# Kernel tuning notes

Hardware: AMD Instinct MI355X
Metric: run time of the kernel (lower is better)

The kernel has to match this reference:

```python
import jax, jax.numpy as jnp
import numpy as np
import math

D = 768
SCALE = math.sqrt(D)


def setup_inputs() -> dict:
    key = jax.random.key(0)
    k1, k2, k3, k4 = jax.random.split(key, 4)
    lhs = jax.random.normal(k1, (8, 1024, D), dtype=jnp.float32)
    rhs = jax.random.normal(k2, (8, 1024, D), dtype=jnp.float32)
    # xavier_normal_ std = sqrt(2/(fan_in+fan_out))
    std = math.sqrt(2.0 / (D + D))
    W_lhs = jax.random.normal(k3, (D, D), dtype=jnp.float32) * std
    W_rhs = jax.random.normal(k4, (D, D), dtype=jnp.float32) * std
    return {"lhs": lhs, "rhs": rhs, "W_lhs": W_lhs, "W_rhs": W_rhs}


def reference(lhs, rhs, W_lhs, W_rhs):
    # Linear (no bias): x @ W.T, then tanh
    l = jnp.tanh(jnp.einsum('nld,ed->nle', lhs, W_lhs))  # (N, L, D)
    r = jnp.tanh(jnp.einsum('nrd,ed->nre', rhs, W_rhs))  # (N, R, D)
    scores = jnp.einsum('nld,nrd->nlr', l, r)            # (N, L, R)
    attn_lhs = jax.nn.softmax(scores, axis=2)            # unscaled, row softmax
    attn_rhs = jax.nn.softmax(scores / SCALE, axis=1)    # scaled, column softmax
    out_lhs = jnp.einsum('nlr,nrd->nld', attn_lhs, rhs)
    out_rhs = jnp.einsum('nlr,nld->nrd', attn_rhs, lhs)
    return (jnp.concatenate([lhs, out_lhs], axis=2),
            jnp.concatenate([rhs, out_rhs], axis=2))
```

## Files before the change

kernel.cpp:

```cpp
#include <hip/hip_runtime.h>

typedef _Float16 f16_t;
typedef _Float16 f16x4 __attribute__((ext_vector_type(4)));
typedef _Float16 f16x8 __attribute__((ext_vector_type(8)));
typedef short s16x8 __attribute__((ext_vector_type(8)));
typedef float floatx4 __attribute__((ext_vector_type(4)));

#define NB 8
#define SEQ 1024
#define DIM 768
#define INV_SCALE 0.03608439182435161f
#define ROW_SHIFT 40.0f

__device__ inline unsigned short f2bf(float f) {
  unsigned u = __builtin_bit_cast(unsigned, f);
  u += 0x7fffu + ((u >> 16) & 1u);
  return (unsigned short)(u >> 16);
}

__device__ inline void async_load16(const void* g, void* l) {
  __builtin_amdgcn_global_load_lds((__attribute__((address_space(1))) void*)g,
                                   (__attribute__((address_space(3))) void*)l,
                                   16, 0, 0);
}


__global__ __launch_bounds__(256, 3) void gemm_proj(
    const f16_t* __restrict__ A0, const f16_t* __restrict__ W0,
    const f16_t* __restrict__ A1, const f16_t* __restrict__ W1,
    f16_t* __restrict__ C0, f16_t* __restrict__ C1) {
  __shared__ __align__(16) f16_t sA[128 * 64];
  __shared__ __align__(16) f16_t sB[128 * 64];
  const int b = blockIdx.x;
  const int n = b & 7;
  const int s = b >> 3;
  const int side = s / 48;
  const int t = s - side * 48;
  const int myb = t / 6, j = t - myb * 6;
  const int my = n * 8 + myb;
  const f16_t* Ab = (side ? A1 : A0) + (size_t)my * 128 * DIM;
  const f16_t* Bb = (side ? W1 : W0) + (size_t)j * 128 * DIM;
  f16_t* C = side ? C1 : C0;
  const int tid = threadIdx.x;
  const int lane = tid & 63;
  const int wave = tid >> 6;
  const int wr = wave >> 1, wc = wave & 1;
  const int fr = lane & 15;
  const int fq = lane >> 4;
  const int swz = ((lane & 7) ^ (lane >> 3)) << 3;
  const int x7 = (fr & 7) << 3;

  floatx4 acc[4][4] = {};

  for (int kt = 0; kt < DIM; kt += 64) {
    #pragma unroll
    for (int i = 0; i < 4; ++i) {
      const int ch = i * 4 + wave;
      const int row = ch * 8 + (lane >> 3);
      const size_t g = (size_t)row * DIM + kt + swz;
      async_load16(Ab + g, (char*)sA + ch * 1024);
      async_load16(Bb + g, (char*)sB + ch * 1024);
    }
    __syncthreads();
    #pragma unroll
    for (int ks = 0; ks < 64; ks += 32) {
      f16x8 af[4], bf[4];
      #pragma unroll
      for (int t2 = 0; t2 < 4; ++t2) {
        const int cs = (ks + fq * 8) ^ x7;
        af[t2] = *(const f16x8*)&sA[(wr * 64 + t2 * 16 + fr) * 64 + cs];
        bf[t2] = *(const f16x8*)&sB[(wc * 64 + t2 * 16 + fr) * 64 + cs];
      }
      #pragma unroll
      for (int ti = 0; ti < 4; ++ti)
        #pragma unroll
        for (int tj = 0; tj < 4; ++tj)
          acc[ti][tj] = __builtin_amdgcn_mfma_f32_16x16x32_f16(
              af[ti], bf[tj], acc[ti][tj], 0, 0, 0);
    }
    __syncthreads();
  }

  const size_t m0 = (size_t)my * 128, n0 = (size_t)j * 128;
  #pragma unroll
  for (int ti = 0; ti < 4; ++ti)
    #pragma unroll
    for (int tj = 0; tj < 4; ++tj) {
      const size_t gm = m0 + wr * 64 + ti * 16 + fq * 4;
      const size_t gn = n0 + wc * 64 + tj * 16 + fr;
      #pragma unroll
      for (int i = 0; i < 4; ++i) {
        const float e = __expf(2.f * acc[ti][tj][i]);
        C[(gm + i) * DIM + gn] =
            (f16_t)(1.f - 2.f * __builtin_amdgcn_rcpf(e + 1.f));
      }
    }
}

__global__ __launch_bounds__(256, 3) void scores_mix(
    const f16_t* __restrict__ A, const f16_t* __restrict__ B,
    const float* __restrict__ lhs32, const float* __restrict__ rhs32,
    unsigned short* __restrict__ e_l, f16_t* __restrict__ e_rT,
    f16_t* __restrict__ lhsT, unsigned short* __restrict__ rhsT,
    float* __restrict__ rowpart, float* __restrict__ colpart) {
  __shared__ __align__(16) char smem[32768];
  const int b = blockIdx.x;
  const int tid = threadIdx.x;

  if (b >= 512) {
    float(*tile)[65] = (float(*)[65])smem;
    const int t = b - 512;
    const int side = t >> 7;
    const int n = (t >> 4) & 7, r0 = (t & 15) * 64;
    const float* in = (side ? rhs32 : lhs32) + (size_t)n * SEQ * DIM;
    const int x = tid & 63, y = tid >> 6;
    for (int d0 = 0; d0 < DIM; d0 += 64) {
      #pragma unroll
      for (int yy = y; yy < 64; yy += 4)
        tile[yy][x] = in[(size_t)(r0 + yy) * DIM + d0 + x];
      __syncthreads();
      if (side == 0) {
        f16_t* out = lhsT + (size_t)n * SEQ * DIM;
        #pragma unroll
        for (int yy = y; yy < 64; yy += 4)
          out[(size_t)(d0 + yy) * SEQ + r0 + x] = (f16_t)tile[x][yy];
      } else {
        unsigned short* out = rhsT + (size_t)n * SEQ * DIM;
        #pragma unroll
        for (int yy = y; yy < 64; yy += 4)
          out[(size_t)(d0 + yy) * SEQ + r0 + x] = f2bf(tile[x][yy]);
      }
      __syncthreads();
    }
    return;
  }

  f16_t* sA = (f16_t*)smem;
  f16_t* sB = sA + 8192;
  const int z = b & 7;
  const int s = b >> 3;
  const int my = s >> 3, j = s & 7;
  const f16_t* Ab = A + (size_t)z * SEQ * DIM + (size_t)my * 128 * DIM;
  const f16_t* Bb = B + (size_t)z * SEQ * DIM + (size_t)j * 128 * DIM;
  const int lane = tid & 63;
  const int wave = tid >> 6;
  const int wr = wave >> 1, wc = wave & 1;
  const int fr = lane & 15;
  const int fq = lane >> 4;
  const int swz = ((lane & 7) ^ (lane >> 3)) << 3;
  const int x7 = (fr & 7) << 3;

  floatx4 acc[4][4] = {};

  for (int kt = 0; kt < DIM; kt += 64) {
    #pragma unroll
    for (int i = 0; i < 4; ++i) {
      const int ch = i * 4 + wave;
      const int row = ch * 8 + (lane >> 3);
      const size_t g = (size_t)row * DIM + kt + swz;
      async_load16(Ab + g, (char*)sA + ch * 1024);
      async_load16(Bb + g, (char*)sB + ch * 1024);
    }
    __syncthreads();
    #pragma unroll
    for (int ks = 0; ks < 64; ks += 32) {
      f16x8 af[4], bf[4];
      #pragma unroll
      for (int t2 = 0; t2 < 4; ++t2) {
        const int cs = (ks + fq * 8) ^ x7;
        af[t2] = *(const f16x8*)&sA[(wr * 64 + t2 * 16 + fr) * 64 + cs];
        bf[t2] = *(const f16x8*)&sB[(wc * 64 + t2 * 16 + fr) * 64 + cs];
      }
      #pragma unroll
      for (int ti = 0; ti < 4; ++ti)
        #pragma unroll
        for (int tj = 0; tj < 4; ++tj)
          acc[ti][tj] = __builtin_amdgcn_mfma_f32_16x16x32_f16(
              af[ti], bf[tj], acc[ti][tj], 0, 0, 0);
    }
    __syncthreads();
  }

  const size_t m0 = (size_t)my * 128, n0 = (size_t)j * 128;
  unsigned short* eL = e_l + (size_t)z * SEQ * SEQ;
  f16_t* eT = e_rT + (size_t)z * SEQ * SEQ;

  #pragma unroll
  for (int ti = 0; ti < 4; ++ti) {
    #pragma unroll
    for (int i = 0; i < 4; ++i) {
      const int rloc = wr * 64 + ti * 16 + fq * 4 + i;
      float sum = 0.f;
      #pragma unroll
      for (int tj = 0; tj < 4; ++tj) {
        const float e = __expf(acc[ti][tj][i] - ROW_SHIFT);
        sum += e;
        eL[(m0 + rloc) * SEQ + n0 + wc * 64 + tj * 16 + fr] = f2bf(e);
      }
      sum += __shfl_xor(sum, 1, 64);
      sum += __shfl_xor(sum, 2, 64);
      sum += __shfl_xor(sum, 4, 64);
      sum += __shfl_xor(sum, 8, 64);
      if (fr == 0)
        rowpart[((size_t)(z * 16 + j * 2 + wc)) * SEQ + m0 + rloc] = sum;
    }
  }
  #pragma unroll
  for (int tj = 0; tj < 4; ++tj) {
    const int rp = wc * 64 + tj * 16 + fr;
    float sum = 0.f;
    #pragma unroll
    for (int ti = 0; ti < 4; ++ti) {
      #pragma unroll
      for (int i = 0; i < 4; ++i) {
        const float e = __expf(acc[ti][tj][i] * INV_SCALE);
        sum += e;
        const int cp = wr * 64 + ti * 16 + fq * 4 + i;
        *(f16_t*)(smem + rp * 256 + ((cp * 2) ^ ((rp & 7) << 4))) = (f16_t)e;
      }
    }
    sum += __shfl_xor(sum, 16, 64);
    sum += __shfl_xor(sum, 32, 64);
    if (fq == 0)
      colpart[((size_t)(z * 16 + my * 2 + wr)) * SEQ + n0 + rp] = sum;
  }
  __syncthreads();
  #pragma unroll
  for (int it = 0; it < 8; ++it) {
    const int r = it * 16 + (tid >> 4), chunk = tid & 15;
    const f16x8 v =
        *(const f16x8*)(smem + r * 256 + ((chunk * 16) ^ ((r & 7) << 4)));
    *(f16x8*)&eT[(n0 + r) * SEQ + m0 + chunk * 8] = v;
  }
}

template <bool BF>
__device__ __forceinline__ void apply_body(
    const f16_t* __restrict__ Ab, const f16_t* __restrict__ Bb,
    float* __restrict__ C, const float* __restrict__ pp, f16_t* sA, f16_t* sB,
    float* sinv) {
  const int tid = threadIdx.x;
  const int lane = tid & 63;
  const int wave = tid >> 6;
  const int wr = wave >> 1, wc = wave & 1;
  const int fr = lane & 15;
  const int fq = lane >> 4;
  const int swz = ((lane & 7) ^ (lane >> 3)) << 3;
  const int x7 = (fr & 7) << 3;

  if (tid < 128) {
    float s = 0.f;
    #pragma unroll
    for (int k = 0; k < 16; ++k) s += pp[k * SEQ + tid];
    sinv[tid] = 1.f / s;
  }

  floatx4 acc[4][4] = {};

  for (int kt = 0; kt < SEQ; kt += 64) {
    #pragma unroll
    for (int i = 0; i < 4; ++i) {
      const int ch = i * 4 + wave;
      const int row = ch * 8 + (lane >> 3);
      const size_t g = (size_t)row * SEQ + kt + swz;
      async_load16(Ab + g, (char*)sA + ch * 1024);
      async_load16(Bb + g, (char*)sB + ch * 1024);
    }
    __syncthreads();
    #pragma unroll
    for (int ks = 0; ks < 64; ks += 32) {
      const int cs = (ks + fq * 8) ^ x7;
      #pragma unroll
      for (int ti = 0; ti < 4; ++ti) {
        const f16_t* pa = &sA[(wr * 64 + ti * 16 + fr) * 64 + cs];
        #pragma unroll
        for (int tj = 0; tj < 4; ++tj) {
          const f16_t* pb = &sB[(wc * 64 + tj * 16 + fr) * 64 + cs];
          if constexpr (BF)
            acc[ti][tj] = __builtin_amdgcn_mfma_f32_16x16x32_bf16(
                *(const s16x8*)pa, *(const s16x8*)pb, acc[ti][tj], 0, 0, 0);
          else
            acc[ti][tj] = __builtin_amdgcn_mfma_f32_16x16x32_f16(
                *(const f16x8*)pa, *(const f16x8*)pb, acc[ti][tj], 0, 0, 0);
        }
      }
    }
    __syncthreads();
  }

  #pragma unroll
  for (int ti = 0; ti < 4; ++ti) {
    const int gm = wr * 64 + ti * 16 + fq * 4;
    const floatx4 iv = *(const floatx4*)&sinv[gm];
    #pragma unroll
    for (int tj = 0; tj < 4; ++tj) {
      const int gn = wc * 64 + tj * 16 + fr;
      #pragma unroll
      for (int i = 0; i < 4; ++i)
        C[(size_t)(gm + i) * (2 * DIM) + gn] = acc[ti][tj][i] * iv[i];
    }
  }
}

__global__ __launch_bounds__(256, 3) void gemm_apply(
    const f16_t* __restrict__ e_l, const f16_t* __restrict__ e_rT,
    const f16_t* __restrict__ rhsT, const f16_t* __restrict__ lhsT,
    const float* __restrict__ rowpart, const float* __restrict__ colpart,
    float* __restrict__ out0, float* __restrict__ out1) {
  __shared__ __align__(16) f16_t sA[128 * 64];
  __shared__ __align__(16) f16_t sB[128 * 64];
  __shared__ __align__(16) float sinv[128];
  const int b = blockIdx.x;
  const int n = b & 7;
  const int s = b >> 3;
  const int side = s / 48;
  const int t = s - side * 48;
  const int my = t / 6, j = t - my * 6;
  const size_t m0 = (size_t)my * 128, n0 = (size_t)j * 128;
  if (side == 0) {
    apply_body<true>(e_l + (size_t)n * SEQ * SEQ + m0 * SEQ,
                     rhsT + (size_t)n * SEQ * DIM + n0 * SEQ,
                     out0 + (size_t)n * SEQ * 2 * DIM + DIM + m0 * 2 * DIM + n0,
                     rowpart + (size_t)n * 16 * SEQ + m0, sA, sB, sinv);
  } else {
    apply_body<false>(
        e_rT + (size_t)n * SEQ * SEQ + m0 * SEQ,
        lhsT + (size_t)n * SEQ * DIM + n0 * SEQ,
        out1 + (size_t)n * SEQ * 2 * DIM + DIM + m0 * 2 * DIM + n0,
        colpart + (size_t)n * 16 * SEQ + m0, sA, sB, sinv);
  }
}

__global__ __launch_bounds__(256) void prep(
    const float* __restrict__ lhs, const float* __restrict__ rhs,
    const float* __restrict__ Wl, const float* __restrict__ Wr,
    f16_t* __restrict__ lf, f16_t* __restrict__ rf, f16_t* __restrict__ Wlh,
    f16_t* __restrict__ Wrh, float* __restrict__ o0, float* __restrict__ o1) {
  const int which = blockIdx.y;
  const int bx = blockIdx.x;
  if (bx >= 6144) {
    const float4* in = (const float4*)(which ? Wr : Wl);
    f16_t* out = which ? Wrh : Wlh;
    const int idx = (bx - 6144) * 256 + threadIdx.x;
    const float4 v = in[idx];
    f16x4 h = {(f16_t)v.x, (f16_t)v.y, (f16_t)v.z, (f16_t)v.w};
    *(f16x4*)(out + idx * 4) = h;
    return;
  }
  const float4* in = (const float4*)(which ? rhs : lhs);
  f16_t* out = which ? rf : lf;
  float* outh = which ? o1 : o0;
  const int idx = bx * 256 + threadIdx.x;
  const float4 v = in[idx];
  const int i4 = idx * 4;
  f16x4 h = {(f16_t)v.x, (f16_t)v.y, (f16_t)v.z, (f16_t)v.w};
  *(f16x4*)(out + i4) = h;
  const int row = i4 / DIM, col = i4 % DIM;
  *(float4*)&outh[(size_t)row * (2 * DIM) + col] = v;
}

extern "C" void kernel_launch(void* const* d_in, const int* in_sizes, int n_in,
                              void* d_out, int out_size, void* d_ws,
                              size_t ws_size, hipStream_t stream) {
  const float* lhs = (const float*)d_in[0];
  const float* rhs = (const float*)d_in[1];
  const float* Wl = (const float*)d_in[2];
  const float* Wr = (const float*)d_in[3];
  float* out0 = (float*)d_out;
  float* out1 = out0 + (size_t)NB * SEQ * (2 * DIM);

  char* ws = (char*)d_ws;
  f16_t* lhsT = (f16_t*)(ws + 0);
  unsigned short* rhsT = (unsigned short*)(ws + 12582912);
  f16_t* l_f = (f16_t*)(ws + 25165824);
  f16_t* r_f = (f16_t*)(ws + 37748736);
  f16_t* lhs_f = (f16_t*)(ws + 50331648);
  f16_t* rhs_f = (f16_t*)(ws + 62914560);
  f16_t* Wl_h = (f16_t*)(ws + 75497472);
  f16_t* Wr_h = (f16_t*)(ws + 76677120);
  unsigned short* e_l = (unsigned short*)(ws + 50331648);
  f16_t* e_rT = (f16_t*)(ws + 67108864);
  float* rowpart = (float*)(ws + 83886080);
  float* colpart = (float*)(ws + 84410368);

  prep<<<dim3(6720, 2), 256, 0, stream>>>(lhs, rhs, Wl, Wr, lhs_f, rhs_f,
                                          Wl_h, Wr_h, out0, out1);
  gemm_proj<<<768, 256, 0, stream>>>(lhs_f, Wl_h, rhs_f, Wr_h, l_f, r_f);
  scores_mix<<<768, 256, 0, stream>>>(l_f, r_f, lhs, rhs, e_l, e_rT, lhsT,
                                      rhsT, rowpart, colpart);
  gemm_apply<<<768, 256, 0, stream>>>((const f16_t*)e_l, e_rT,
                                      (const f16_t*)rhsT, lhsT, rowpart,
                                      colpart, out0, out1);
}
```

Before: 242.8 us.

## Fuse fp32-to-fp16 conversion into projection GEMM and drop prep kernel

The separate prep kernel, which converted inputs and weights to fp16 and copied the passthrough halves of the outputs, is removed. The projection GEMM now loads fp32 tiles directly with vector loads, converts them in registers and writes swizzled fp16 into LDS. The passthrough copy moves into the transpose blocks of scores_mix. This removes one launch and a full fp16 round trip through memory. In exchange the GEMM loses its async global-to-LDS loads, reads twice as many bytes per tile, and spends extra VALU work on conversion.

```diff
diff --git a/kernel.cpp b/kernel.cpp
--- a/kernel.cpp
+++ b/kernel.cpp
@@ -26,8 +26,8 @@
 
 
 __global__ __launch_bounds__(256, 3) void gemm_proj(
-    const f16_t* __restrict__ A0, const f16_t* __restrict__ W0,
-    const f16_t* __restrict__ A1, const f16_t* __restrict__ W1,
+    const float* __restrict__ A0, const float* __restrict__ W0,
+    const float* __restrict__ A1, const float* __restrict__ W1,
     f16_t* __restrict__ C0, f16_t* __restrict__ C1) {
   __shared__ __align__(16) f16_t sA[128 * 64];
   __shared__ __align__(16) f16_t sB[128 * 64];
@@ -38,8 +38,8 @@
   const int t = s - side * 48;
   const int myb = t / 6, j = t - myb * 6;
   const int my = n * 8 + myb;
-  const f16_t* Ab = (side ? A1 : A0) + (size_t)my * 128 * DIM;
-  const f16_t* Bb = (side ? W1 : W0) + (size_t)j * 128 * DIM;
+  const float* Ab = (side ? A1 : A0) + (size_t)my * 128 * DIM;
+  const float* Bb = (side ? W1 : W0) + (size_t)j * 128 * DIM;
   f16_t* C = side ? C1 : C0;
   const int tid = threadIdx.x;
   const int lane = tid & 63;
@@ -47,19 +47,24 @@
   const int wr = wave >> 1, wc = wave & 1;
   const int fr = lane & 15;
   const int fq = lane >> 4;
-  const int swz = ((lane & 7) ^ (lane >> 3)) << 3;
   const int x7 = (fr & 7) << 3;
+  const int c4 = tid & 15;
+  const int rq = tid >> 4;
 
   floatx4 acc[4][4] = {};
 
   for (int kt = 0; kt < DIM; kt += 64) {
     #pragma unroll
-    for (int i = 0; i < 4; ++i) {
-      const int ch = i * 4 + wave;
-      const int row = ch * 8 + (lane >> 3);
-      const size_t g = (size_t)row * DIM + kt + swz;
-      async_load16(Ab + g, (char*)sA + ch * 1024);
-      async_load16(Bb + g, (char*)sB + ch * 1024);
+    for (int p = 0; p < 8; ++p) {
+      const int row = p * 16 + rq;
+      const int dst =
+          row * 64 + (((c4 >> 1) ^ (row & 7)) << 3) + ((c4 & 1) << 2);
+      const float4 va = *(const float4*)&Ab[(size_t)row * DIM + kt + c4 * 4];
+      const float4 vb = *(const float4*)&Bb[(size_t)row * DIM + kt + c4 * 4];
+      *(f16x4*)&sA[dst] =
+          f16x4{(f16_t)va.x, (f16_t)va.y, (f16_t)va.z, (f16_t)va.w};
+      *(f16x4*)&sB[dst] =
+          f16x4{(f16_t)vb.x, (f16_t)vb.y, (f16_t)vb.z, (f16_t)vb.w};
     }
     __syncthreads();
     #pragma unroll
@@ -102,7 +107,8 @@
     const float* __restrict__ lhs32, const float* __restrict__ rhs32,
     unsigned short* __restrict__ e_l, f16_t* __restrict__ e_rT,
     f16_t* __restrict__ lhsT, unsigned short* __restrict__ rhsT,
-    float* __restrict__ rowpart, float* __restrict__ colpart) {
+    float* __restrict__ rowpart, float* __restrict__ colpart,
+    float* __restrict__ out0, float* __restrict__ out1) {
   __shared__ __align__(16) char smem[32768];
   const int b = blockIdx.x;
   const int tid = threadIdx.x;
@@ -113,11 +119,15 @@
     const int side = t >> 7;
     const int n = (t >> 4) & 7, r0 = (t & 15) * 64;
     const float* in = (side ? rhs32 : lhs32) + (size_t)n * SEQ * DIM;
+    float* oh = (side ? out1 : out0) + (size_t)n * SEQ * 2 * DIM;
     const int x = tid & 63, y = tid >> 6;
     for (int d0 = 0; d0 < DIM; d0 += 64) {
       #pragma unroll
-      for (int yy = y; yy < 64; yy += 4)
-        tile[yy][x] = in[(size_t)(r0 + yy) * DIM + d0 + x];
+      for (int yy = y; yy < 64; yy += 4) {
+        const float v = in[(size_t)(r0 + yy) * DIM + d0 + x];
+        tile[yy][x] = v;
+        oh[(size_t)(r0 + yy) * (2 * DIM) + d0 + x] = v;
+      }
       __syncthreads();
       if (side == 0) {
         f16_t* out = lhsT + (size_t)n * SEQ * DIM;
@@ -331,34 +341,6 @@
   }
 }
 
-__global__ __launch_bounds__(256) void prep(
-    const float* __restrict__ lhs, const float* __restrict__ rhs,
-    const float* __restrict__ Wl, const float* __restrict__ Wr,
-    f16_t* __restrict__ lf, f16_t* __restrict__ rf, f16_t* __restrict__ Wlh,
-    f16_t* __restrict__ Wrh, float* __restrict__ o0, float* __restrict__ o1) {
-  const int which = blockIdx.y;
-  const int bx = blockIdx.x;
-  if (bx >= 6144) {
-    const float4* in = (const float4*)(which ? Wr : Wl);
-    f16_t* out = which ? Wrh : Wlh;
-    const int idx = (bx - 6144) * 256 + threadIdx.x;
-    const float4 v = in[idx];
-    f16x4 h = {(f16_t)v.x, (f16_t)v.y, (f16_t)v.z, (f16_t)v.w};
-    *(f16x4*)(out + idx * 4) = h;
-    return;
-  }
-  const float4* in = (const float4*)(which ? rhs : lhs);
-  f16_t* out = which ? rf : lf;
-  float* outh = which ? o1 : o0;
-  const int idx = bx * 256 + threadIdx.x;
-  const float4 v = in[idx];
-  const int i4 = idx * 4;
-  f16x4 h = {(f16_t)v.x, (f16_t)v.y, (f16_t)v.z, (f16_t)v.w};
-  *(f16x4*)(out + i4) = h;
-  const int row = i4 / DIM, col = i4 % DIM;
-  *(float4*)&outh[(size_t)row * (2 * DIM) + col] = v;
-}
-
 extern "C" void kernel_launch(void* const* d_in, const int* in_sizes, int n_in,
                               void* d_out, int out_size, void* d_ws,
                               size_t ws_size, hipStream_t stream) {
@@ -374,20 +356,14 @@
   unsigned short* rhsT = (unsigned short*)(ws + 12582912);
   f16_t* l_f = (f16_t*)(ws + 25165824);
   f16_t* r_f = (f16_t*)(ws + 37748736);
-  f16_t* lhs_f = (f16_t*)(ws + 50331648);
-  f16_t* rhs_f = (f16_t*)(ws + 62914560);
-  f16_t* Wl_h = (f16_t*)(ws + 75497472);
-  f16_t* Wr_h = (f16_t*)(ws + 76677120);
   unsigned short* e_l = (unsigned short*)(ws + 50331648);
   f16_t* e_rT = (f16_t*)(ws + 67108864);
   float* rowpart = (float*)(ws + 83886080);
   float* colpart = (float*)(ws + 84410368);
 
-  prep<<<dim3(6720, 2), 256, 0, stream>>>(lhs, rhs, Wl, Wr, lhs_f, rhs_f,
-                                          Wl_h, Wr_h, out0, out1);
-  gemm_proj<<<768, 256, 0, stream>>>(lhs_f, Wl_h, rhs_f, Wr_h, l_f, r_f);
+  gemm_proj<<<768, 256, 0, stream>>>(lhs, Wl, rhs, Wr, l_f, r_f);
   scores_mix<<<768, 256, 0, stream>>>(l_f, r_f, lhs, rhs, e_l, e_rT, lhsT,
-                                      rhsT, rowpart, colpart);
+                                      rhsT, rowpart, colpart, out0, out1);
   gemm_apply<<<768, 256, 0, stream>>>((const f16_t*)e_l, e_rT,
                                       (const f16_t*)rhsT, lhsT, rowpart,
                                       colpart, out0, out1);
```

Measured after the change: 267.1 us. 1.1x slower.

## Fuse input transposes into prep kernel and reorder GEMM tile mapping

Applied to the files above, without the earlier changes.

Folds the lhs/rhs transpose (to fp16 and bf16 transposed copies) into the prep kernel, so each fp32 input is read once instead of twice. Prep now works on 64x64 tiles with a padded shared-memory tile. The scores kernel becomes a pure GEMM launched with fewer blocks. Block indexing in the projection and apply kernels now makes consecutive blocks share the same column tile, which should improve cache reuse of the weight and B operands. The cost is a heavier prep kernel with shared-memory transposes and the loss of the overlap the transpose previously had with the scores GEMM.

```diff
diff --git a/kernel.cpp b/kernel.cpp
--- a/kernel.cpp
+++ b/kernel.cpp
@@ -4,6 +4,7 @@
 typedef _Float16 f16x4 __attribute__((ext_vector_type(4)));
 typedef _Float16 f16x8 __attribute__((ext_vector_type(8)));
 typedef short s16x8 __attribute__((ext_vector_type(8)));
+typedef unsigned short u16x4 __attribute__((ext_vector_type(4)));
 typedef float floatx4 __attribute__((ext_vector_type(4)));
 
 #define NB 8
@@ -24,6 +25,68 @@
                                    16, 0, 0);
 }
 
+
+__global__ __launch_bounds__(256) void prep(
+    const float* __restrict__ lhs, const float* __restrict__ rhs,
+    const float* __restrict__ Wl, const float* __restrict__ Wr,
+    f16_t* __restrict__ lf, f16_t* __restrict__ rf, f16_t* __restrict__ lhsT,
+    unsigned short* __restrict__ rhsT, f16_t* __restrict__ Wlh,
+    f16_t* __restrict__ Wrh, float* __restrict__ o0, float* __restrict__ o1) {
+  const int z = blockIdx.z;
+  const int tid = threadIdx.x;
+  const int x4 = (tid & 15) * 4, ty = tid >> 4;
+  const int c0 = blockIdx.x * 64, r0 = blockIdx.y * 64;
+  if (z >= 16) {
+    if (blockIdx.y >= 12) return;
+    const float* in = (z == 17 ? Wr : Wl);
+    f16_t* out = (z == 17 ? Wrh : Wlh);
+    #pragma unroll
+    for (int it = 0; it < 4; ++it) {
+      const int row = r0 + ty + it * 16;
+      const float4 v = *(const float4*)&in[(size_t)row * DIM + c0 + x4];
+      f16x4 h = {(f16_t)v.x, (f16_t)v.y, (f16_t)v.z, (f16_t)v.w};
+      *(f16x4*)&out[(size_t)row * DIM + c0 + x4] = h;
+    }
+    return;
+  }
+  __shared__ float tile[64][65];
+  const int n = z & 7;
+  const float* in = (z < 8 ? lhs : rhs) + (size_t)n * SEQ * DIM;
+  f16_t* fout = (z < 8 ? lf : rf) + (size_t)n * SEQ * DIM;
+  float* oh = (z < 8 ? o0 : o1) + (size_t)n * SEQ * 2 * DIM;
+  #pragma unroll
+  for (int it = 0; it < 4; ++it) {
+    const int row = ty + it * 16;
+    const float4 v = *(const float4*)&in[(size_t)(r0 + row) * DIM + c0 + x4];
+    f16x4 h = {(f16_t)v.x, (f16_t)v.y, (f16_t)v.z, (f16_t)v.w};
+    *(f16x4*)&fout[(size_t)(r0 + row) * DIM + c0 + x4] = h;
+    *(float4*)&oh[(size_t)(r0 + row) * 2 * DIM + c0 + x4] = v;
+    tile[row][x4 + 0] = v.x;
+    tile[row][x4 + 1] = v.y;
+    tile[row][x4 + 2] = v.z;
+    tile[row][x4 + 3] = v.w;
+  }
+  __syncthreads();
+  if (z < 8) {
+    f16_t* T = lhsT + (size_t)n * SEQ * DIM;
+    #pragma unroll
+    for (int it = 0; it < 4; ++it) {
+      const int cr = ty + it * 16;
+      f16x4 o = {(f16_t)tile[x4 + 0][cr], (f16_t)tile[x4 + 1][cr],
+                 (f16_t)tile[x4 + 2][cr], (f16_t)tile[x4 + 3][cr]};
+      *(f16x4*)&T[(size_t)(c0 + cr) * SEQ + r0 + x4] = o;
+    }
+  } else {
+    unsigned short* T = rhsT + (size_t)n * SEQ * DIM;
+    #pragma unroll
+    for (int it = 0; it < 4; ++it) {
+      const int cr = ty + it * 16;
+      u16x4 o = {f2bf(tile[x4 + 0][cr]), f2bf(tile[x4 + 1][cr]),
+                 f2bf(tile[x4 + 2][cr]), f2bf(tile[x4 + 3][cr])};
+      *(u16x4*)&T[(size_t)(c0 + cr) * SEQ + r0 + x4] = o;
+    }
+  }
+}
 
 __global__ __launch_bounds__(256, 3) void gemm_proj(
     const f16_t* __restrict__ A0, const f16_t* __restrict__ W0,
@@ -36,7 +99,7 @@
   const int s = b >> 3;
   const int side = s / 48;
   const int t = s - side * 48;
-  const int myb = t / 6, j = t - myb * 6;
+  const int j = t >> 3, myb = t & 7;
   const int my = n * 8 + myb;
   const f16_t* Ab = (side ? A1 : A0) + (size_t)my * 128 * DIM;
   const f16_t* Bb = (side ? W1 : W0) + (size_t)j * 128 * DIM;
@@ -97,44 +160,13 @@
     }
 }
 
-__global__ __launch_bounds__(256, 3) void scores_mix(
+__global__ __launch_bounds__(256, 3) void gemm_scores(
     const f16_t* __restrict__ A, const f16_t* __restrict__ B,
-    const float* __restrict__ lhs32, const float* __restrict__ rhs32,
     unsigned short* __restrict__ e_l, f16_t* __restrict__ e_rT,
-    f16_t* __restrict__ lhsT, unsigned short* __restrict__ rhsT,
     float* __restrict__ rowpart, float* __restrict__ colpart) {
   __shared__ __align__(16) char smem[32768];
   const int b = blockIdx.x;
   const int tid = threadIdx.x;
-
-  if (b >= 512) {
-    float(*tile)[65] = (float(*)[65])smem;
-    const int t = b - 512;
-    const int side = t >> 7;
-    const int n = (t >> 4) & 7, r0 = (t & 15) * 64;
-    const float* in = (side ? rhs32 : lhs32) + (size_t)n * SEQ * DIM;
-    const int x = tid & 63, y = tid >> 6;
-    for (int d0 = 0; d0 < DIM; d0 += 64) {
-      #pragma unroll
-      for (int yy = y; yy < 64; yy += 4)
-        tile[yy][x] = in[(size_t)(r0 + yy) * DIM + d0 + x];
-      __syncthreads();
-      if (side == 0) {
-        f16_t* out = lhsT + (size_t)n * SEQ * DIM;
-        #pragma unroll
-        for (int yy = y; yy < 64; yy += 4)
-          out[(size_t)(d0 + yy) * SEQ + r0 + x] = (f16_t)tile[x][yy];
-      } else {
-        unsigned short* out = rhsT + (size_t)n * SEQ * DIM;
-        #pragma unroll
-        for (int yy = y; yy < 64; yy += 4)
-          out[(size_t)(d0 + yy) * SEQ + r0 + x] = f2bf(tile[x][yy]);
-      }
-      __syncthreads();
-    }
-    return;
-  }
-
   f16_t* sA = (f16_t*)smem;
   f16_t* sB = sA + 8192;
   const int z = b & 7;
@@ -315,7 +347,7 @@
   const int s = b >> 3;
   const int side = s / 48;
   const int t = s - side * 48;
-  const int my = t / 6, j = t - my * 6;
+  const int j = t >> 3, my = t & 7;
   const size_t m0 = (size_t)my * 128, n0 = (size_t)j * 128;
   if (side == 0) {
     apply_body<true>(e_l + (size_t)n * SEQ * SEQ + m0 * SEQ,
@@ -329,34 +361,6 @@
         out1 + (size_t)n * SEQ * 2 * DIM + DIM + m0 * 2 * DIM + n0,
         colpart + (size_t)n * 16 * SEQ + m0, sA, sB, sinv);
   }
-}
-
-__global__ __launch_bounds__(256) void prep(
-    const float* __restrict__ lhs, const float* __restrict__ rhs,
-    const float* __restrict__ Wl, const float* __restrict__ Wr,
-    f16_t* __restrict__ lf, f16_t* __restrict__ rf, f16_t* __restrict__ Wlh,
-    f16_t* __restrict__ Wrh, float* __restrict__ o0, float* __restrict__ o1) {
-  const int which = blockIdx.y;
-  const int bx = blockIdx.x;
-  if (bx >= 6144) {
-    const float4* in = (const float4*)(which ? Wr : Wl);
-    f16_t* out = which ? Wrh : Wlh;
-    const int idx = (bx - 6144) * 256 + threadIdx.x;
-    const float4 v = in[idx];
-    f16x4 h = {(f16_t)v.x, (f16_t)v.y, (f16_t)v.z, (f16_t)v.w};
-    *(f16x4*)(out + idx * 4) = h;
-    return;
-  }
-  const float4* in = (const float4*)(which ? rhs : lhs);
-  f16_t* out = which ? rf : lf;
-  float* outh = which ? o1 : o0;
-  const int idx = bx * 256 + threadIdx.x;
-  const float4 v = in[idx];
-  const int i4 = idx * 4;
-  f16x4 h = {(f16_t)v.x, (f16_t)v.y, (f16_t)v.z, (f16_t)v.w};
-  *(f16x4*)(out + i4) = h;
-  const int row = i4 / DIM, col = i4 % DIM;
-  *(float4*)&outh[(size_t)row * (2 * DIM) + col] = v;
 }
 
 extern "C" void kernel_launch(void* const* d_in, const int* in_sizes, int n_in,
@@ -383,11 +387,11 @@
   float* rowpart = (float*)(ws + 83886080);
   float* colpart = (float*)(ws + 84410368);
 
-  prep<<<dim3(6720, 2), 256, 0, stream>>>(lhs, rhs, Wl, Wr, lhs_f, rhs_f,
-                                          Wl_h, Wr_h, out0, out1);
+  prep<<<dim3(12, 16, 18), 256, 0, stream>>>(lhs, rhs, Wl, Wr, lhs_f, rhs_f,
+                                             lhsT, rhsT, Wl_h, Wr_h, out0,
+                                             out1);
   gemm_proj<<<768, 256, 0, stream>>>(lhs_f, Wl_h, rhs_f, Wr_h, l_f, r_f);
-  scores_mix<<<768, 256, 0, stream>>>(l_f, r_f, lhs, rhs, e_l, e_rT, lhsT,
-                                      rhsT, rowpart, colpart);
+  gemm_scores<<<512, 256, 0, stream>>>(l_f, r_f, e_l, e_rT, rowpart, colpart);
   gemm_apply<<<768, 256, 0, stream>>>((const f16_t*)e_l, e_rT,
                                       (const f16_t*)rhsT, lhsT, rowpart,
                                       colpart, out0, out1);
```

New measurement: 233.9 us. -3.6%, faster.
